# Optimization experiments

Hardware: AMD Instinct MI355X
Metric: run time of the kernel (lower is better)

Reference implementation:

```python
import jax, jax.numpy as jnp
import numpy as np

B, N, C, K = 16, 1024, 192, 9
H = 4 * C  # hidden of second MLP pair


def _gelu(x):
    return jax.nn.gelu(x, approximate=False)  # torch nn.GELU default is exact erf


def _mlp(x, w1, b1, w2, b2):
    # TwoLayerNN: Linear -> GELU -> Linear
    return _gelu(x @ w1.T + b1) @ w2.T + b2


def _linear_init(key, out_d, in_d):
    k1, k2 = jax.random.split(key)
    s = 1.0 / np.sqrt(in_d)
    w = jax.random.uniform(k1, (out_d, in_d), minval=-s, maxval=s, dtype=jnp.float32)
    b = jax.random.uniform(k2, (out_d,), minval=-s, maxval=s, dtype=jnp.float32)
    return w, b


def setup_inputs() -> dict:
    key = jax.random.key(0)
    ks = jax.random.split(key, 10)
    x = jax.random.normal(ks[0], (B, N, C), dtype=jnp.float32)
    il1_w1, il1_b1 = _linear_init(ks[1], C, C)
    il1_w2, il1_b2 = _linear_init(ks[2], C, C)
    ol1_w1, ol1_b1 = _linear_init(ks[3], C, C)
    ol1_w2, ol1_b2 = _linear_init(ks[4], C, C)
    il2_w1, il2_b1 = _linear_init(ks[5], H, C)
    il2_w2, il2_b2 = _linear_init(ks[6], C, H)
    ol2_w1, ol2_b1 = _linear_init(ks[7], H, C)
    ol2_w2, ol2_b2 = _linear_init(ks[8], C, H)
    fc_w, fc_b = _linear_init(ks[9], C, 2 * C)  # Conv1d(2C, C, 1) == Linear(2C->C)
    return dict(x=x,
                il1_w1=il1_w1, il1_b1=il1_b1, il1_w2=il1_w2, il1_b2=il1_b2,
                fc_w=fc_w, fc_b=fc_b,
                ol1_w1=ol1_w1, ol1_b1=ol1_b1, ol1_w2=ol1_w2, ol1_b2=ol1_b2,
                il2_w1=il2_w1, il2_b1=il2_b1, il2_w2=il2_w2, il2_b2=il2_b2,
                ol2_w1=ol2_w1, ol2_b1=ol2_b1, ol2_w2=ol2_w2, ol2_b2=ol2_b2)


def reference(x, il1_w1, il1_b1, il1_w2, il1_b2, fc_w, fc_b,
              ol1_w1, ol1_b1, ol1_w2, ol1_b2,
              il2_w1, il2_b1, il2_w2, il2_b2,
              ol2_w1, ol2_b1, ol2_w2, ol2_b2):
    Bx, Nx, Cx = x.shape
    # 1) dense similarity + KNN graph (indices only; no grad path through sim)
    sim = jnp.einsum('bnc,bmc->bnm', x, x)                       # [B,N,N]
    _, graph = jax.lax.top_k(sim, K)                             # [B,N,K] int32
    shortcut = x
    # 2) node transform then gather-max aggregation
    h = _mlp(x.reshape(Bx * Nx, Cx), il1_w1, il1_b1, il1_w2, il1_b2).reshape(Bx, Nx, Cx)
    nb = jnp.take_along_axis(h[:, None, :, :], graph[:, :, :, None], axis=2)  # [B,N,K,C]
    agg = jnp.max(nb - h[:, :, None, :], axis=2)                 # [B,N,C]
    # 3) stack along new last dim then flatten -> interleaved channels [x_c0,agg_c0,x_c1,...]
    cat = jnp.stack([h, agg], axis=-1).reshape(Bx, Nx, 2 * Cx)   # [B,N,2C]
    h = cat @ fc_w.T + fc_b                                      # Conv1d k=1 == Linear
    h = _mlp(_gelu(h).reshape(Bx * Nx, Cx), ol1_w1, ol1_b1, ol1_w2, ol1_b2).reshape(Bx, Nx, Cx)
    x1 = h + shortcut
    # 4) FFN block (two TwoLayerNNs with external GELU between them)
    f = _mlp(x1.reshape(Bx * Nx, Cx), il2_w1, il2_b1, il2_w2, il2_b2)
    f = _mlp(_gelu(f), ol2_w1, ol2_b1, ol2_w2, ol2_b2).reshape(Bx, Nx, Cx)
    return f + x1
```

## Files before the change

kernel.cpp:

```cpp
#include <hip/hip_runtime.h>
#include <hip/hip_bf16.h>
#include <math.h>

#define DEVINL __device__ __forceinline__

typedef __attribute__((ext_vector_type(4))) float f32x4;
typedef __attribute__((ext_vector_type(8))) short s16x8;

DEVINL unsigned short f2bf(float f) {
  union { float f; unsigned u; } v; v.f = f;
  unsigned r = v.u + 0x7FFFu + ((v.u >> 16) & 1u);
  return (unsigned short)(r >> 16);
}
DEVINL float bf2f(unsigned short s) {
  union { unsigned u; float f; } v; v.u = ((unsigned)s) << 16;
  return v.f;
}
DEVINL float gelu_exact(float x) {
  return 0.5f * x * (1.0f + erff(x * 0.70710678118654752f));
}

__global__ __launch_bounds__(256) void conv_kernel(const float* __restrict__ x,
                                                   unsigned short* __restrict__ xh,
                                                   unsigned short* __restrict__ xl) {
  int i = blockIdx.x * 256 + threadIdx.x;
  float4 v = ((const float4*)x)[i];
  float f[4] = {v.x, v.y, v.z, v.w};
  unsigned short h[4], l[4];
#pragma unroll
  for (int j = 0; j < 4; ++j) {
    h[j] = f2bf(f[j]);
    l[j] = f2bf(f[j] - bf2f(h[j]));
  }
  uint2 uh, ul;
  uh.x = (unsigned)h[0] | ((unsigned)h[1] << 16);
  uh.y = (unsigned)h[2] | ((unsigned)h[3] << 16);
  ul.x = (unsigned)l[0] | ((unsigned)l[1] << 16);
  ul.y = (unsigned)l[2] | ((unsigned)l[3] << 16);
  ((uint2*)xh)[i] = uh;
  ((uint2*)xl)[i] = ul;
}

struct WArgs {
  const float* s[9];
  unsigned short* d[9];
  int n4[9];
};
__global__ __launch_bounds__(256) void wconv_kernel(WArgs a) {
  int seg = blockIdx.y;
  int i = blockIdx.x * 256 + threadIdx.x;
  if (i >= a.n4[seg]) return;
  float4 v = ((const float4*)a.s[seg])[i];
  float f[4] = {v.x, v.y, v.z, v.w};
  uint2 u;
  u.x = (unsigned)f2bf(f[0]) | ((unsigned)f2bf(f[1]) << 16);
  u.y = (unsigned)f2bf(f[2]) | ((unsigned)f2bf(f[3]) << 16);
  ((uint2*)a.d[seg])[i] = u;
}

__global__ __launch_bounds__(512)
#if __has_attribute(amdgpu_waves_per_eu)
__attribute__((amdgpu_waves_per_eu(2, 4)))
#endif
void simtopk_kernel(const unsigned short* __restrict__ xh,
                    const unsigned short* __restrict__ xl,
                    int* __restrict__ graph) {
  const int tid  = threadIdx.x;
  const int lane = tid & 63;
  const int w    = tid >> 6;
  const int wm   = w >> 1, wn = w & 1;

  const int lin  = blockIdx.y * 16 + blockIdx.x;
  const int work = (lin & 7) * 32 + (lin >> 3);
  const int rb   = work & 15;
  const int b    = work >> 4;

  __shared__ float Lv[512 * 9];
  __shared__ int   Li[512 * 9];
  __shared__ float Mv[256 * 9];
  __shared__ int   Mi[256 * 9];

  const unsigned short* xhb = xh + (size_t)b * (1024 * 192);
  const unsigned short* xlb = xl + (size_t)b * (1024 * 192);

  s16x8 ah[6], al[6];
#pragma unroll
  for (int ks = 0; ks < 6; ++ks) {
    int r = rb * 64 + wm * 16 + (lane & 15);
    size_t off = (size_t)r * 192 + ks * 32 + (lane >> 4) * 8;
    ah[ks] = *(const s16x8*)(xhb + off);
    al[ks] = *(const s16x8*)(xlb + off);
  }

  float tv[9]; int tix[9];
#pragma unroll
  for (int k = 0; k < 9; ++k) { tv[k] = -3.0e38f; tix[k] = 1 << 30; }

  for (int ct = 0; ct < 16; ++ct) {
    const size_t tbase = (size_t)(ct * 64) * 192;
    f32x4 a0[2], a1[2], a2[2];
#pragma unroll
    for (int n2 = 0; n2 < 2; ++n2) { a0[n2] = 0; a1[n2] = 0; a2[n2] = 0; }

#pragma unroll
    for (int ks = 0; ks < 6; ++ks) {
      const int koff = ks * 32 + (lane >> 4) * 8;
#pragma unroll
      for (int n2 = 0; n2 < 2; ++n2) {
        const int rc = (wn * 2 + n2) * 16 + (lane & 15);
        const size_t g = tbase + (size_t)rc * 192 + koff;
        s16x8 bh = *(const s16x8*)(xhb + g);
        s16x8 bl = *(const s16x8*)(xlb + g);
        a0[n2] = __builtin_amdgcn_mfma_f32_16x16x32_bf16(bh, ah[ks], a0[n2], 0, 0, 0);
        a1[n2] = __builtin_amdgcn_mfma_f32_16x16x32_bf16(bl, ah[ks], a1[n2], 0, 0, 0);
        a2[n2] = __builtin_amdgcn_mfma_f32_16x16x32_bf16(bh, al[ks], a2[n2], 0, 0, 0);
      }
    }

#pragma unroll
    for (int n2 = 0; n2 < 2; ++n2) {
      int cbase = ct * 64 + (wn * 2 + n2) * 16 + (lane >> 4) * 4;
#pragma unroll
      for (int r = 0; r < 4; ++r) {
        float v = a0[n2][r] + a1[n2][r] + a2[n2][r];
        int   c = cbase + r;
        if (v > tv[8]) {
          tv[8] = v; tix[8] = c;
#pragma unroll
          for (int s = 8; s > 0; --s) {
            if (tv[s] > tv[s - 1]) {
              float fv = tv[s]; tv[s] = tv[s - 1]; tv[s - 1] = fv;
              int   fi = tix[s]; tix[s] = tix[s - 1]; tix[s - 1] = fi;
            }
          }
        }
      }
    }
  }

  {
    int rowloc = wm * 16 + (lane & 15);
    int listid = wn * 4 + (lane >> 4);
    int lbase  = (rowloc * 8 + listid) * 9;
#pragma unroll
    for (int k = 0; k < 9; ++k) { Lv[lbase + k] = tv[k]; Li[lbase + k] = tix[k]; }
  }
  __syncthreads();

  if (tid < 256) {
    int r = tid >> 2, p = tid & 3;
    float fv[9]; int fi[9];
#pragma unroll
    for (int k = 0; k < 9; ++k) { fv[k] = -3.0e38f; fi[k] = 1 << 30; }
    for (int s2 = 0; s2 < 2; ++s2) {
      int base = (r * 8 + p * 2 + s2) * 9;
#pragma unroll
      for (int k = 0; k < 9; ++k) {
        float v = Lv[base + k]; int c = Li[base + k];
        bool better = (v > fv[8]) || (v == fv[8] && c < fi[8]);
        if (better) {
          fv[8] = v; fi[8] = c;
#pragma unroll
          for (int s = 8; s > 0; --s) {
            bool up = (fv[s] > fv[s - 1]) || (fv[s] == fv[s - 1] && fi[s] < fi[s - 1]);
            if (up) {
              float a = fv[s]; fv[s] = fv[s - 1]; fv[s - 1] = a;
              int  ii = fi[s]; fi[s] = fi[s - 1]; fi[s - 1] = ii;
            }
          }
        }
      }
    }
#pragma unroll
    for (int k = 0; k < 9; ++k) { Mv[tid * 9 + k] = fv[k]; Mi[tid * 9 + k] = fi[k]; }
  }
  __syncthreads();

  if (tid < 64) {
    float fv[9]; int fi[9];
#pragma unroll
    for (int k = 0; k < 9; ++k) { fv[k] = -3.0e38f; fi[k] = 1 << 30; }
    for (int p = 0; p < 4; ++p) {
      int base = (tid * 4 + p) * 9;
#pragma unroll
      for (int k = 0; k < 9; ++k) {
        float v = Mv[base + k]; int c = Mi[base + k];
        bool better = (v > fv[8]) || (v == fv[8] && c < fi[8]);
        if (better) {
          fv[8] = v; fi[8] = c;
#pragma unroll
          for (int s = 8; s > 0; --s) {
            bool up = (fv[s] > fv[s - 1]) || (fv[s] == fv[s - 1] && fi[s] < fi[s - 1]);
            if (up) {
              float a = fv[s]; fv[s] = fv[s - 1]; fv[s - 1] = a;
              int  ii = fi[s]; fi[s] = fi[s - 1]; fi[s - 1] = ii;
            }
          }
        }
      }
    }
    int* gout = graph + ((size_t)b * 1024 + rb * 64 + tid) * 9;
#pragma unroll
    for (int k = 0; k < 9; ++k) gout[k] = fi[k];
  }
}

__global__ __launch_bounds__(256) void agg_kernel(const unsigned short* __restrict__ h,
                                                  const int* __restrict__ graph,
                                                  unsigned short* __restrict__ cat) {
  int gid  = blockIdx.x * 4 + (threadIdx.x >> 6);
  int lane = threadIdx.x & 63;
  int b = gid >> 10;
  int n = gid & 1023;
  const unsigned short* hb = h + (size_t)b * (1024 * 192);
  const int* g = graph + (size_t)gid * 9;
  float hn[3];
#pragma unroll
  for (int j = 0; j < 3; ++j) hn[j] = bf2f(hb[(size_t)n * 192 + lane + j * 64]);
  float ag[3] = {-3.0e38f, -3.0e38f, -3.0e38f};
  for (int k = 0; k < 9; ++k) {
    int idx = g[k];
#pragma unroll
    for (int j = 0; j < 3; ++j) {
      float v = bf2f(hb[(size_t)idx * 192 + lane + j * 64]) - hn[j];
      ag[j] = fmaxf(ag[j], v);
    }
  }
  unsigned* crow = (unsigned*)cat + (size_t)gid * 192;
#pragma unroll
  for (int j = 0; j < 3; ++j) {
    int c = lane + j * 64;
    crow[c] = (unsigned)f2bf(hn[j]) | ((unsigned)f2bf(ag[j]) << 16);
  }
}

template <bool GELU_, bool RESID>
__global__ __launch_bounds__(256) void gemm_kernel(const unsigned short* __restrict__ A,
                                                   const unsigned short* __restrict__ W,
                                                   const float* __restrict__ bias,
                                                   const float* __restrict__ resid,
                                                   unsigned short* __restrict__ outb,
                                                   float* __restrict__ outf,
                                                   int N, int K) {
  __shared__ unsigned short As[2][128 * 64];
  __shared__ unsigned short Ws[2][64 * 64];

  const int tid  = threadIdx.x;
  const int lane = tid & 63;
  const int w    = tid >> 6;
  const int m0   = blockIdx.x * 128;
  const int n0   = blockIdx.y * 64;

  auto stageA = [&](int buf, int kt) {
#pragma unroll
    for (int i = 0; i < 4; ++i) {
      int chunk = w * 4 + i;
      int row = chunk * 8 + (lane >> 3);
      const unsigned short* src = A + (size_t)(m0 + row) * K + kt * 64
                                    + (((lane & 7) ^ (row & 7)) * 8);
      unsigned short* dst = &As[buf][chunk * 512];
      __builtin_amdgcn_global_load_lds((const __attribute__((address_space(1))) void*)src,
                                       (__attribute__((address_space(3))) void*)dst, 16, 0, 0);
    }
  };
  auto stageW = [&](int buf, int kt) {
#pragma unroll
    for (int i = 0; i < 2; ++i) {
      int chunk = w * 2 + i;
      int row = chunk * 8 + (lane >> 3);
      const unsigned short* src = W + (size_t)(n0 + row) * K + kt * 64
                                    + (((lane & 7) ^ (row & 7)) * 8);
      unsigned short* dst = &Ws[buf][chunk * 512];
      __builtin_amdgcn_global_load_lds((const __attribute__((address_space(1))) void*)src,
                                       (__attribute__((address_space(3))) void*)dst, 16, 0, 0);
    }
  };

  stageA(0, 0);
  stageW(0, 0);
  __syncthreads();

  const int wm = w >> 1, wn = w & 1;
  f32x4 acc[4][2];
#pragma unroll
  for (int a = 0; a < 4; ++a)
#pragma unroll
    for (int c = 0; c < 2; ++c) acc[a][c] = 0;

  const int nk = K >> 6;
  for (int kt = 0; kt < nk; ++kt) {
    const int cur = kt & 1;
    if (kt + 1 < nk) { stageA(cur ^ 1, kt + 1); stageW(cur ^ 1, kt + 1); }
#pragma unroll
    for (int ks = 0; ks < 2; ++ks) {
      const int kc = ks * 4 + (lane >> 4);
      s16x8 af[4], bfr[2];
#pragma unroll
      for (int m2 = 0; m2 < 4; ++m2) {
        int row = wm * 64 + m2 * 16 + (lane & 15);
        af[m2] = *(const s16x8*)&As[cur][row * 64 + ((kc ^ (row & 7)) * 8)];
      }
#pragma unroll
      for (int n2 = 0; n2 < 2; ++n2) {
        int rw = wn * 32 + n2 * 16 + (lane & 15);
        bfr[n2] = *(const s16x8*)&Ws[cur][rw * 64 + ((kc ^ (rw & 7)) * 8)];
      }
#pragma unroll
      for (int m2 = 0; m2 < 4; ++m2)
#pragma unroll
        for (int n2 = 0; n2 < 2; ++n2)
          acc[m2][n2] = __builtin_amdgcn_mfma_f32_16x16x32_bf16(af[m2], bfr[n2], acc[m2][n2], 0, 0, 0);
    }
    __syncthreads();
  }

#pragma unroll
  for (int m2 = 0; m2 < 4; ++m2)
#pragma unroll
    for (int n2 = 0; n2 < 2; ++n2)
#pragma unroll
      for (int r = 0; r < 4; ++r) {
        int row = m0 + wm * 64 + m2 * 16 + (lane >> 4) * 4 + r;
        int col = n0 + wn * 32 + n2 * 16 + (lane & 15);
        float v = acc[m2][n2][r] + bias[col];
        if (GELU_) v = gelu_exact(v);
        if (RESID) v += resid[(size_t)row * N + col];
        size_t o = (size_t)row * N + col;
        if (outb) outb[o] = f2bf(v);
        if (outf) outf[o] = v;
      }
}

extern "C" void kernel_launch(void* const* d_in, const int* in_sizes, int n_in,
                              void* d_out, int out_size, void* d_ws, size_t ws_size,
                              hipStream_t stream) {
  (void)in_sizes; (void)n_in; (void)out_size; (void)ws_size;
  const float* x      = (const float*)d_in[0];
  const float* il1_w1 = (const float*)d_in[1];
  const float* il1_b1 = (const float*)d_in[2];
  const float* il1_w2 = (const float*)d_in[3];
  const float* il1_b2 = (const float*)d_in[4];
  const float* fc_w   = (const float*)d_in[5];
  const float* fc_b   = (const float*)d_in[6];
  const float* ol1_w1 = (const float*)d_in[7];
  const float* ol1_b1 = (const float*)d_in[8];
  const float* ol1_w2 = (const float*)d_in[9];
  const float* ol1_b2 = (const float*)d_in[10];
  const float* il2_w1 = (const float*)d_in[11];
  const float* il2_b1 = (const float*)d_in[12];
  const float* il2_w2 = (const float*)d_in[13];
  const float* il2_b2 = (const float*)d_in[14];
  const float* ol2_w1 = (const float*)d_in[15];
  const float* ol2_b1 = (const float*)d_in[16];
  const float* ol2_w2 = (const float*)d_in[17];
  const float* ol2_b2 = (const float*)d_in[18];

  char* ws = (char*)d_ws;
  const size_t SZ = 16384ull * 192 * 2;
  unsigned short* xbf  = (unsigned short*)(ws);
  unsigned short* t13  = (unsigned short*)(ws + SZ);
  unsigned short* hbuf = (unsigned short*)(ws + 2 * SZ);
  unsigned short* t2   = (unsigned short*)(ws + 3 * SZ);
  unsigned short* x1b  = (unsigned short*)(ws + 4 * SZ);
  unsigned short* catg = (unsigned short*)(ws + 5 * SZ);
  float*          x1f  = (float*)(ws + 7 * SZ);
  unsigned short* uv   = (unsigned short*)(ws + 9 * SZ);
  unsigned short* xlo  = uv;
  int*            graph = (int*)(ws + 13 * SZ);
  unsigned short* wb   = (unsigned short*)(ws + 13 * SZ + (1 << 20));

  unsigned short* il1_w1b = wb;
  unsigned short* il1_w2b = wb + 36864;
  unsigned short* fcb     = wb + 73728;
  unsigned short* ol1_w1b = wb + 147456;
  unsigned short* ol1_w2b = wb + 184320;
  unsigned short* il2_w1b = wb + 221184;
  unsigned short* il2_w2b = wb + 368640;
  unsigned short* ol2_w1b = wb + 516096;
  unsigned short* ol2_w2b = wb + 663552;

  WArgs wa;
  wa.s[0] = il1_w1; wa.d[0] = il1_w1b; wa.n4[0] = 36864 / 4;
  wa.s[1] = il1_w2; wa.d[1] = il1_w2b; wa.n4[1] = 36864 / 4;
  wa.s[2] = fc_w;   wa.d[2] = fcb;     wa.n4[2] = 73728 / 4;
  wa.s[3] = ol1_w1; wa.d[3] = ol1_w1b; wa.n4[3] = 36864 / 4;
  wa.s[4] = ol1_w2; wa.d[4] = ol1_w2b; wa.n4[4] = 36864 / 4;
  wa.s[5] = il2_w1; wa.d[5] = il2_w1b; wa.n4[5] = 147456 / 4;
  wa.s[6] = il2_w2; wa.d[6] = il2_w2b; wa.n4[6] = 147456 / 4;
  wa.s[7] = ol2_w1; wa.d[7] = ol2_w1b; wa.n4[7] = 147456 / 4;
  wa.s[8] = ol2_w2; wa.d[8] = ol2_w2b; wa.n4[8] = 147456 / 4;

  conv_kernel<<<3072, 256, 0, stream>>>(x, xbf, xlo);
  wconv_kernel<<<dim3(144, 9), 256, 0, stream>>>(wa);
  simtopk_kernel<<<dim3(16, 16), 512, 0, stream>>>(xbf, xlo, graph);
  gemm_kernel<true,  false><<<dim3(128, 3), 256, 0, stream>>>(xbf, il1_w1b, il1_b1, nullptr, t13, nullptr, 192, 192);
  gemm_kernel<false, false><<<dim3(128, 3), 256, 0, stream>>>(t13, il1_w2b, il1_b2, nullptr, hbuf, nullptr, 192, 192);
  agg_kernel<<<4096, 256, 0, stream>>>(hbuf, graph, catg);
  gemm_kernel<true,  false><<<dim3(128, 3), 256, 0, stream>>>(catg, fcb, fc_b, nullptr, t2, nullptr, 192, 384);
  gemm_kernel<true,  false><<<dim3(128, 3), 256, 0, stream>>>(t2, ol1_w1b, ol1_b1, nullptr, t13, nullptr, 192, 192);
  gemm_kernel<false, true ><<<dim3(128, 3), 256, 0, stream>>>(t13, ol1_w2b, ol1_b2, x, x1b, x1f, 192, 192);
  gemm_kernel<true,  false><<<dim3(128, 12), 256, 0, stream>>>(x1b, il2_w1b, il2_b1, nullptr, uv, nullptr, 768, 192);
  gemm_kernel<true,  false><<<dim3(128, 3), 256, 0, stream>>>(uv, il2_w2b, il2_b2, nullptr, catg, nullptr, 192, 768);
  gemm_kernel<true,  false><<<dim3(128, 12), 256, 0, stream>>>(catg, ol2_w1b, ol2_b1, nullptr, uv, nullptr, 768, 192);
  gemm_kernel<false, true ><<<dim3(128, 3), 256, 0, stream>>>(uv, ol2_w2b, ol2_b2, x1f, nullptr, (float*)d_out, 192, 768);
}
```

Baseline: 273.0 us.

## Double-buffer B-operand loads in similarity top-k loop with register prefetch

Restructures the similarity/top-k main loop into 32 sub-tiles of 16 columns, with two register buffers so that global loads for the next sub-tile are issued before the MFMA and top-k insertion work on the current one. Scheduling barriers keep the compiler from interleaving or reordering the loads and compute. The waves-per-EU hint is tightened to 2 to give the doubled register buffers room. The goal is to hide global load latency, at the cost of higher register pressure and lower occupancy.

```diff
diff --git a/kernel.cpp b/kernel.cpp
--- a/kernel.cpp
+++ b/kernel.cpp
@@ -60,7 +60,7 @@
 
 __global__ __launch_bounds__(512)
 #if __has_attribute(amdgpu_waves_per_eu)
-__attribute__((amdgpu_waves_per_eu(2, 4)))
+__attribute__((amdgpu_waves_per_eu(2, 2)))
 #endif
 void simtopk_kernel(const unsigned short* __restrict__ xh,
                     const unsigned short* __restrict__ xl,
@@ -83,11 +83,14 @@
   const unsigned short* xhb = xh + (size_t)b * (1024 * 192);
   const unsigned short* xlb = xl + (size_t)b * (1024 * 192);
 
+  const int rlane = lane & 15;
+  const int koffb = (lane >> 4) * 8;
+
   s16x8 ah[6], al[6];
 #pragma unroll
   for (int ks = 0; ks < 6; ++ks) {
-    int r = rb * 64 + wm * 16 + (lane & 15);
-    size_t off = (size_t)r * 192 + ks * 32 + (lane >> 4) * 8;
+    int r = rb * 64 + wm * 16 + rlane;
+    size_t off = (size_t)r * 192 + ks * 32 + koffb;
     ah[ks] = *(const s16x8*)(xhb + off);
     al[ks] = *(const s16x8*)(xlb + off);
   }
@@ -96,50 +99,60 @@
 #pragma unroll
   for (int k = 0; k < 9; ++k) { tv[k] = -3.0e38f; tix[k] = 1 << 30; }
 
-  for (int ct = 0; ct < 16; ++ct) {
-    const size_t tbase = (size_t)(ct * 64) * 192;
-    f32x4 a0[2], a1[2], a2[2];
-#pragma unroll
-    for (int n2 = 0; n2 < 2; ++n2) { a0[n2] = 0; a1[n2] = 0; a2[n2] = 0; }
-
-#pragma unroll
-    for (int ks = 0; ks < 6; ++ks) {
-      const int koff = ks * 32 + (lane >> 4) * 8;
-#pragma unroll
-      for (int n2 = 0; n2 < 2; ++n2) {
-        const int rc = (wn * 2 + n2) * 16 + (lane & 15);
-        const size_t g = tbase + (size_t)rc * 192 + koff;
-        s16x8 bh = *(const s16x8*)(xhb + g);
-        s16x8 bl = *(const s16x8*)(xlb + g);
-        a0[n2] = __builtin_amdgcn_mfma_f32_16x16x32_bf16(bh, ah[ks], a0[n2], 0, 0, 0);
-        a1[n2] = __builtin_amdgcn_mfma_f32_16x16x32_bf16(bl, ah[ks], a1[n2], 0, 0, 0);
-        a2[n2] = __builtin_amdgcn_mfma_f32_16x16x32_bf16(bh, al[ks], a2[n2], 0, 0, 0);
-      }
-    }
-
-#pragma unroll
-    for (int n2 = 0; n2 < 2; ++n2) {
-      int cbase = ct * 64 + (wn * 2 + n2) * 16 + (lane >> 4) * 4;
-#pragma unroll
-      for (int r = 0; r < 4; ++r) {
-        float v = a0[n2][r] + a1[n2][r] + a2[n2][r];
-        int   c = cbase + r;
-        if (v > tv[8]) {
-          tv[8] = v; tix[8] = c;
-#pragma unroll
-          for (int s = 8; s > 0; --s) {
-            if (tv[s] > tv[s - 1]) {
-              float fv = tv[s]; tv[s] = tv[s - 1]; tv[s - 1] = fv;
-              int   fi = tix[s]; tix[s] = tix[s - 1]; tix[s - 1] = fi;
-            }
-          }
-        }
-      }
-    }
-  }
+#define ST_PREFETCH(CC, BH, BL)                                                \
+  if ((CC) < 32) {                                                             \
+    const int colb_ = (((CC) >> 1) * 64) + wn * 32 + (((CC) & 1) * 16);        \
+    const size_t ro_ = (size_t)(colb_ + rlane) * 192 + koffb;                  \
+    _Pragma("unroll")                                                          \
+    for (int ks = 0; ks < 6; ++ks) {                                           \
+      (BH)[ks] = *(const s16x8*)(xhb + ro_ + ks * 32);                         \
+      (BL)[ks] = *(const s16x8*)(xlb + ro_ + ks * 32);                         \
+    }                                                                          \
+  }
+
+#define ST_COMPUTE(CC, BH, BL)                                                 \
+  {                                                                            \
+    f32x4 a0 = 0, a1 = 0, a2 = 0;                                             \
+    _Pragma("unroll")                                                          \
+    for (int ks = 0; ks < 6; ++ks) {                                           \
+      a0 = __builtin_amdgcn_mfma_f32_16x16x32_bf16((BH)[ks], ah[ks], a0, 0, 0, 0); \
+      a1 = __builtin_amdgcn_mfma_f32_16x16x32_bf16((BL)[ks], ah[ks], a1, 0, 0, 0); \
+      a2 = __builtin_amdgcn_mfma_f32_16x16x32_bf16((BH)[ks], al[ks], a2, 0, 0, 0); \
+    }                                                                          \
+    const int colb_ = (((CC) >> 1) * 64) + wn * 32 + (((CC) & 1) * 16);        \
+    const int cbase_ = colb_ + (lane >> 4) * 4;                                \
+    _Pragma("unroll")                                                          \
+    for (int r = 0; r < 4; ++r) {                                              \
+      float v = a0[r] + a1[r] + a2[r];                                         \
+      int   c = cbase_ + r;                                                    \
+      if (v > tv[8]) {                                                         \
+        tv[8] = v; tix[8] = c;                                                 \
+        _Pragma("unroll")                                                      \
+        for (int s = 8; s > 0; --s) {                                          \
+          if (tv[s] > tv[s - 1]) {                                             \
+            float fv = tv[s]; tv[s] = tv[s - 1]; tv[s - 1] = fv;               \
+            int   fi = tix[s]; tix[s] = tix[s - 1]; tix[s - 1] = fi;           \
+          }                                                                    \
+        }                                                                      \
+      }                                                                        \
+    }                                                                          \
+  }
+
+  s16x8 Abh[6], Abl[6], Bbh[6], Bbl[6];
+  ST_PREFETCH(0, Abh, Abl);
+  for (int cc = 0; cc < 32; cc += 2) {
+    ST_PREFETCH(cc + 1, Bbh, Bbl);
+    __builtin_amdgcn_sched_barrier(0);
+    ST_COMPUTE(cc, Abh, Abl);
+    ST_PREFETCH(cc + 2, Abh, Abl);
+    __builtin_amdgcn_sched_barrier(0);
+    ST_COMPUTE(cc + 1, Bbh, Bbl);
+  }
+#undef ST_PREFETCH
+#undef ST_COMPUTE
 
   {
-    int rowloc = wm * 16 + (lane & 15);
+    int rowloc = wm * 16 + rlane;
     int listid = wn * 4 + (lane >> 4);
     int lbase  = (rowloc * 8 + listid) * 9;
 #pragma unroll
```

After: 273.1 us. About the same (+0.0%).

## Restructure similarity top-k into 16-row blocks with LDS-staged query rows

Applied to the files above, without the earlier changes.

The similarity+top-k kernel now launches 1024 blocks of 256 threads instead of 256 blocks of 512. Each block handles 16 query rows, which are staged in swizzled shared memory, and each wave sweeps 256 candidate columns. This raises grid parallelism and cuts per-thread register pressure (no 12 resident A fragments). The cost is that each block re-reads all candidate rows from global memory/L2, which multiplies candidate traffic by four, and the merge tree gets smaller.

```diff
diff --git a/kernel.cpp b/kernel.cpp
--- a/kernel.cpp
+++ b/kernel.cpp
@@ -58,102 +58,92 @@
   ((uint2*)a.d[seg])[i] = u;
 }
 
-__global__ __launch_bounds__(512)
-#if __has_attribute(amdgpu_waves_per_eu)
-__attribute__((amdgpu_waves_per_eu(2, 4)))
-#endif
-void simtopk_kernel(const unsigned short* __restrict__ xh,
-                    const unsigned short* __restrict__ xl,
-                    int* __restrict__ graph) {
-  const int tid  = threadIdx.x;
-  const int lane = tid & 63;
-  const int w    = tid >> 6;
-  const int wm   = w >> 1, wn = w & 1;
-
-  const int lin  = blockIdx.y * 16 + blockIdx.x;
-  const int work = (lin & 7) * 32 + (lin >> 3);
-  const int rb   = work & 15;
-  const int b    = work >> 4;
-
-  __shared__ float Lv[512 * 9];
-  __shared__ int   Li[512 * 9];
-  __shared__ float Mv[256 * 9];
-  __shared__ int   Mi[256 * 9];
+__global__ __launch_bounds__(256) void simtopk_kernel(const unsigned short* __restrict__ xh,
+                                                      const unsigned short* __restrict__ xl,
+                                                      int* __restrict__ graph) {
+  const int tid   = threadIdx.x;
+  const int lane  = tid & 63;
+  const int w     = tid >> 6;
+  const int myrow = lane & 15;
+  const int kq    = lane >> 4;
+
+  const int lin  = blockIdx.x;
+  const int work = (lin & 7) * 128 + (lin >> 3);
+  const int b    = work >> 6;
+  const int rg   = work & 63;
+
+  __shared__ __align__(16) char smem[23040];
+  unsigned short* rowsH = (unsigned short*)smem;
+  unsigned short* rowsL = (unsigned short*)(smem + 6144);
+  float* Lv = (float*)smem;
+  int*   Li = (int*)(smem + 9216);
+  float* Mv = (float*)(smem + 18432);
+  int*   Mi = (int*)(smem + 20736);
 
   const unsigned short* xhb = xh + (size_t)b * (1024 * 192);
   const unsigned short* xlb = xl + (size_t)b * (1024 * 192);
 
-  s16x8 ah[6], al[6];
-#pragma unroll
-  for (int ks = 0; ks < 6; ++ks) {
-    int r = rb * 64 + wm * 16 + (lane & 15);
-    size_t off = (size_t)r * 192 + ks * 32 + (lane >> 4) * 8;
-    ah[ks] = *(const s16x8*)(xhb + off);
-    al[ks] = *(const s16x8*)(xlb + off);
-  }
+  for (int i = tid; i < 384; i += 256) {
+    int r = i / 24, j = i - (i / 24) * 24;
+    size_t g = (size_t)(rg * 16 + r) * 192 + (size_t)j * 8;
+    int dpos = (r * 24 + (j ^ (r & 7))) * 8;
+    *(s16x8*)&rowsH[dpos] = *(const s16x8*)(xhb + g);
+    *(s16x8*)&rowsL[dpos] = *(const s16x8*)(xlb + g);
+  }
+  __syncthreads();
 
   float tv[9]; int tix[9];
 #pragma unroll
   for (int k = 0; k < 9; ++k) { tv[k] = -3.0e38f; tix[k] = 1 << 30; }
 
-  for (int ct = 0; ct < 16; ++ct) {
-    const size_t tbase = (size_t)(ct * 64) * 192;
-    f32x4 a0[2], a1[2], a2[2];
-#pragma unroll
-    for (int n2 = 0; n2 < 2; ++n2) { a0[n2] = 0; a1[n2] = 0; a2[n2] = 0; }
-
+  for (int cc = 0; cc < 16; ++cc) {
+    const int colbase = w * 256 + cc * 16;
+    f32x4 a0 = 0, a1 = 0, a2 = 0;
 #pragma unroll
     for (int ks = 0; ks < 6; ++ks) {
-      const int koff = ks * 32 + (lane >> 4) * 8;
-#pragma unroll
-      for (int n2 = 0; n2 < 2; ++n2) {
-        const int rc = (wn * 2 + n2) * 16 + (lane & 15);
-        const size_t g = tbase + (size_t)rc * 192 + koff;
-        s16x8 bh = *(const s16x8*)(xhb + g);
-        s16x8 bl = *(const s16x8*)(xlb + g);
-        a0[n2] = __builtin_amdgcn_mfma_f32_16x16x32_bf16(bh, ah[ks], a0[n2], 0, 0, 0);
-        a1[n2] = __builtin_amdgcn_mfma_f32_16x16x32_bf16(bl, ah[ks], a1[n2], 0, 0, 0);
-        a2[n2] = __builtin_amdgcn_mfma_f32_16x16x32_bf16(bh, al[ks], a2[n2], 0, 0, 0);
-      }
-    }
-
-#pragma unroll
-    for (int n2 = 0; n2 < 2; ++n2) {
-      int cbase = ct * 64 + (wn * 2 + n2) * 16 + (lane >> 4) * 4;
-#pragma unroll
-      for (int r = 0; r < 4; ++r) {
-        float v = a0[n2][r] + a1[n2][r] + a2[n2][r];
-        int   c = cbase + r;
-        if (v > tv[8]) {
-          tv[8] = v; tix[8] = c;
-#pragma unroll
-          for (int s = 8; s > 0; --s) {
-            if (tv[s] > tv[s - 1]) {
-              float fv = tv[s]; tv[s] = tv[s - 1]; tv[s - 1] = fv;
-              int   fi = tix[s]; tix[s] = tix[s - 1]; tix[s - 1] = fi;
-            }
+      const size_t g = (size_t)(colbase + myrow) * 192 + ks * 32 + kq * 8;
+      s16x8 ch = *(const s16x8*)(xhb + g);
+      s16x8 cl = *(const s16x8*)(xlb + g);
+      const int rpos = (myrow * 24 + ((ks * 4 + kq) ^ (myrow & 7))) * 8;
+      s16x8 rh = *(const s16x8*)&rowsH[rpos];
+      s16x8 rl = *(const s16x8*)&rowsL[rpos];
+      a0 = __builtin_amdgcn_mfma_f32_16x16x32_bf16(ch, rh, a0, 0, 0, 0);
+      a1 = __builtin_amdgcn_mfma_f32_16x16x32_bf16(cl, rh, a1, 0, 0, 0);
+      a2 = __builtin_amdgcn_mfma_f32_16x16x32_bf16(ch, rl, a2, 0, 0, 0);
+    }
+    const int cbase = colbase + kq * 4;
+#pragma unroll
+    for (int r = 0; r < 4; ++r) {
+      float v = a0[r] + a1[r] + a2[r];
+      int   c = cbase + r;
+      if (v > tv[8]) {
+        tv[8] = v; tix[8] = c;
+#pragma unroll
+        for (int s = 8; s > 0; --s) {
+          if (tv[s] > tv[s - 1]) {
+            float fv = tv[s]; tv[s] = tv[s - 1]; tv[s - 1] = fv;
+            int   fi = tix[s]; tix[s] = tix[s - 1]; tix[s - 1] = fi;
           }
         }
       }
     }
   }
+  __syncthreads();
 
   {
-    int rowloc = wm * 16 + (lane & 15);
-    int listid = wn * 4 + (lane >> 4);
-    int lbase  = (rowloc * 8 + listid) * 9;
+    int lbase = (myrow * 16 + (w * 4 + kq)) * 9;
 #pragma unroll
     for (int k = 0; k < 9; ++k) { Lv[lbase + k] = tv[k]; Li[lbase + k] = tix[k]; }
   }
   __syncthreads();
 
-  if (tid < 256) {
+  if (tid < 64) {
     int r = tid >> 2, p = tid & 3;
     float fv[9]; int fi[9];
 #pragma unroll
     for (int k = 0; k < 9; ++k) { fv[k] = -3.0e38f; fi[k] = 1 << 30; }
-    for (int s2 = 0; s2 < 2; ++s2) {
-      int base = (r * 8 + p * 2 + s2) * 9;
+    for (int s4 = 0; s4 < 4; ++s4) {
+      int base = (r * 16 + p * 4 + s4) * 9;
 #pragma unroll
       for (int k = 0; k < 9; ++k) {
         float v = Lv[base + k]; int c = Li[base + k];
@@ -176,7 +166,7 @@
   }
   __syncthreads();
 
-  if (tid < 64) {
+  if (tid < 16) {
     float fv[9]; int fi[9];
 #pragma unroll
     for (int k = 0; k < 9; ++k) { fv[k] = -3.0e38f; fi[k] = 1 << 30; }
@@ -199,7 +189,7 @@
         }
       }
     }
-    int* gout = graph + ((size_t)b * 1024 + rb * 64 + tid) * 9;
+    int* gout = graph + ((size_t)b * 1024 + rg * 16 + tid) * 9;
 #pragma unroll
     for (int k = 0; k < 9; ++k) gout[k] = fi[k];
   }
@@ -392,7 +382,7 @@
 
   conv_kernel<<<3072, 256, 0, stream>>>(x, xbf, xlo);
   wconv_kernel<<<dim3(144, 9), 256, 0, stream>>>(wa);
-  simtopk_kernel<<<dim3(16, 16), 512, 0, stream>>>(xbf, xlo, graph);
+  simtopk_kernel<<<1024, 256, 0, stream>>>(xbf, xlo, graph);
   gemm_kernel<true,  false><<<dim3(128, 3), 256, 0, stream>>>(xbf, il1_w1b, il1_b1, nullptr, t13, nullptr, 192, 192);
   gemm_kernel<false, false><<<dim3(128, 3), 256, 0, stream>>>(t13, il1_w2b, il1_b2, nullptr, hbuf, nullptr, 192, 192);
   agg_kernel<<<4096, 256, 0, stream>>>(hbuf, graph, catg);
```

Measured after the change: 337.3 us. 1.24x slower.
